# Optimization experiments

Measured on AMD Instinct MI355X. Metric: run time of the kernel, lower is better.

Reference implementation:

```python
import jax, jax.numpy as jnp
import numpy as np

A, B, NB = 100_000, 200_000, 6      # atoms, directed bonds, max neighbors
FA, FB, H = 133, 147, 256            # atom fdim, bond fdim, hidden
M, DEPTH = 5_000, 4                  # molecules, message-passing depth


def setup_inputs() -> dict:
    key = jax.random.key(0)
    ks = jax.random.split(key, 12)
    f_atoms = jax.random.normal(ks[0], (A, FA), jnp.float32)
    f_bonds = jax.random.normal(ks[1], (B, FB), jnp.float32)
    a2b = jax.random.randint(ks[2], (A, NB), 0, B, dtype=jnp.int32)
    b2a = jax.random.randint(ks[3], (B,), 0, A, dtype=jnp.int32)
    b2revb = jax.random.randint(ks[4], (B,), 0, B, dtype=jnp.int32)
    # weights (bias=False per args.bias, except W_o which always has bias)
    W_ia = jax.random.normal(ks[5], (FA, H), jnp.float32) / np.sqrt(FA)
    W_ib = jax.random.normal(ks[6], (FB, H), jnp.float32) / np.sqrt(FB)
    W_h = jax.random.normal(ks[7], (DEPTH - 1, H, H), jnp.float32) / np.sqrt(H)
    W_o = jax.random.normal(ks[8], (H, H), jnp.float32) / np.sqrt(H)
    b_o = jax.random.normal(ks[9], (H,), jnp.float32) * 0.01
    W_lr = jax.random.normal(ks[10], (3 * H, H), jnp.float32) / np.sqrt(3 * H)
    # ragged molecule sizes summing exactly to A (avg 20 atoms/mol)
    rng = np.random.default_rng(0)
    sizes = (A // M) + rng.integers(-5, 6, M)
    sizes[-1] += A - sizes.sum()
    sizes = jnp.asarray(sizes, jnp.int32)
    return dict(f_atoms=f_atoms, f_bonds=f_bonds, W_ia=W_ia, W_ib=W_ib,
                W_h=W_h, W_o=W_o, b_o=b_o, W_lr=W_lr,
                a2b=a2b, b2a=b2a, b2revb=b2revb, sizes=sizes)


def _sum_max_agg(message_bond, a2b):
    nei = message_bond[a2b]                 # [A, NB, H] gather
    return nei.sum(axis=1) * nei.max(axis=1)


def reference(f_atoms, f_bonds, W_ia, W_ib, W_h, W_o, b_o, W_lr,
              a2b, b2a, b2revb, sizes):
    input_atom = jax.nn.relu(f_atoms @ W_ia)    # [A, H]
    message_atom = input_atom
    input_bond = jax.nn.relu(f_bonds @ W_ib)    # [B, H]
    message_bond = input_bond
    for d in range(DEPTH - 1):
        agg = _sum_max_agg(message_bond, a2b)          # [A, H]
        message_atom = message_atom + agg
        rev = message_bond[b2revb]                     # [B, H]
        message_bond = message_atom[b2a] - rev
        message_bond = jax.nn.relu(input_bond + message_bond @ W_h[d])
        # dropout p=0.0 -> identity
    agg = _sum_max_agg(message_bond, a2b)              # [A, H]
    agg = jnp.concatenate([agg, message_atom, input_atom], axis=1) @ W_lr
    atom_hiddens = jax.nn.relu(agg @ W_o + b_o)        # [A, H]
    # ragged per-molecule mean pooling (a_scope)
    mol_ids = jnp.repeat(jnp.arange(M), sizes, total_repeat_length=A)
    sums = jax.ops.segment_sum(atom_hiddens, mol_ids, num_segments=M)
    mol_vecs = sums / sizes[:, None].astype(atom_hiddens.dtype)
    return mol_vecs                                    # [M, H]
```

## Files before the change

### kernel.cpp

```cpp
#include <hip/hip_runtime.h>


typedef _Float16 f16;
typedef f16 f16x4 __attribute__((ext_vector_type(4)));
typedef f16 f16x8 __attribute__((ext_vector_type(8)));
typedef __attribute__((ext_vector_type(8))) short bh8;
typedef __attribute__((ext_vector_type(4))) float f32x4;

#define MB_SCALE 0.000244140625f
#define MB_INV   4096.0f
#define AGG_INV  16777216.0f

__device__ __forceinline__ unsigned short f2bf_rne(float f) {
    unsigned u = __float_as_uint(f);
    unsigned r = (u + 0x7fffu + ((u >> 16) & 1u)) >> 16;
    return (unsigned short)r;
}
__device__ __forceinline__ float bfu2f(unsigned short u) {
    return __uint_as_float(((unsigned)u) << 16);
}
__device__ __forceinline__ f32x4 mfma16(bh8 a, bh8 b, f32x4 c) {
    return __builtin_amdgcn_mfma_f32_16x16x32_bf16(a, b, c, 0, 0, 0);
}

__global__ __launch_bounds__(256) void wprep_kernel(
    const float* __restrict__ Wia, const float* __restrict__ Wib,
    const float* __restrict__ Wh,  const float* __restrict__ Wlr,
    const float* __restrict__ Wo,  short* __restrict__ ws)
{
    short* WiaT_hi = ws;
    short* WiaT_lo = ws + 40960;
    short* WibT_hi = ws + 81920;
    short* WibT_lo = ws + 122880;
    short* WhT_hi  = ws + 163840;
    short* WhT_lo  = ws + 360448;
    short* WlrT_hi = ws + 557056;
    short* WlrT_lo = ws + 753664;
    short* WoT_hi  = ws + 950272;
    short* WoT_lo  = ws + 1015808;

    int idx = blockIdx.x * 256 + threadIdx.x;
    float v; short *ph, *pl; int o;
    if (idx < 40960) {
        int n = idx / 160, k = idx - n * 160;
        v = (k < 133) ? Wia[(size_t)k * 256 + n] : 0.f;
        ph = WiaT_hi; pl = WiaT_lo; o = idx;
    } else if (idx < 81920) {
        int j = idx - 40960;
        int n = j / 160, k = j - n * 160;
        v = (k < 147) ? Wib[(size_t)k * 256 + n] : 0.f;
        ph = WibT_hi; pl = WibT_lo; o = j;
    } else if (idx < 278528) {
        int j = idx - 81920;
        int d = j >> 16, rem = j & 65535, n = rem >> 8, k = rem & 255;
        v = Wh[(size_t)d * 65536 + (size_t)k * 256 + n];
        ph = WhT_hi; pl = WhT_lo; o = j;
    } else if (idx < 475136) {
        int j = idx - 278528;
        int n = j / 768, k = j - n * 768;
        v = Wlr[(size_t)k * 256 + n];
        ph = WlrT_hi; pl = WlrT_lo; o = j;
    } else if (idx < 540672) {
        int j = idx - 475136;
        int n = j >> 8, k = j & 255;
        v = Wo[(size_t)k * 256 + n];
        ph = WoT_hi; pl = WoT_lo; o = j;
    } else return;
    unsigned short hb = f2bf_rne(v);
    ph[o] = (short)hb;
    pl[o] = (short)f2bf_rne(v - bfu2f(hb));
}

template <int KPAD, int SRC, int EPI>
__global__ __launch_bounds__(512, 4) void mfma_gemm(
    const void* __restrict__ a0, const void* __restrict__ a1,
    const void* __restrict__ a2,
    const short* __restrict__ Bhi, const short* __restrict__ Blo,
    const float* __restrict__ bias, void* __restrict__ outv,
    int M, int Kact)
{
    __shared__ short As_hi[128 * 40];
    __shared__ short As_lo[(SRC == 2) ? 8 : 128 * 40];

    const int tid  = threadIdx.x;
    const int lane = tid & 63;
    const int w    = tid >> 6;
    const int wm   = (w >> 2) * 64;
    const int wn   = (w & 3) * 64;
    const int row0 = blockIdx.x * 128;

    const int sm = tid >> 2;
    const int sk = (tid & 3) * 8;
    const int fm = lane & 15;
    const int fk = (lane >> 4) * 8;

    int grow = row0 + sm; if (grow > M - 1) grow = M - 1;

    f32x4 acc[4][4];
#pragma unroll
    for (int i = 0; i < 4; ++i)
#pragma unroll
        for (int j = 0; j < 4; ++j) {
            f32x4 z = {0.f, 0.f, 0.f, 0.f};
            acc[i][j] = z;
        }

    for (int k0 = 0; k0 < KPAD; k0 += 32) {
        __syncthreads();
        int base = sm * 40 + sk;
        if (SRC == 0) {
            const float* xrow = (const float*)a0 + (size_t)grow * Kact;
            bh8 h0, l0;
#pragma unroll
            for (int j = 0; j < 8; ++j) {
                int kc = k0 + sk + j;
                float v = (kc < Kact) ? xrow[kc] : 0.f;
                unsigned short hb = f2bf_rne(v);
                h0[j] = (short)hb; l0[j] = (short)f2bf_rne(v - bfu2f(hb));
            }
            *(bh8*)&As_hi[base] = h0;
            *(bh8*)&As_lo[base] = l0;
        } else if (SRC == 1) {
            if (k0 < 512) {
                const float* src = (k0 < 256) ? (const float*)a0 : (const float*)a1;
                int kl = k0 & 255;
                const float4* p = (const float4*)(src + (size_t)grow * 256 + kl + sk);
                float va[8];
#pragma unroll
                for (int q = 0; q < 2; ++q) {
                    float4 f = p[q];
                    va[q * 4 + 0] = f.x; va[q * 4 + 1] = f.y;
                    va[q * 4 + 2] = f.z; va[q * 4 + 3] = f.w;
                }
                bh8 h0, l0;
#pragma unroll
                for (int j = 0; j < 8; ++j) {
                    unsigned short hb = f2bf_rne(va[j]);
                    h0[j] = (short)hb; l0[j] = (short)f2bf_rne(va[j] - bfu2f(hb));
                }
                *(bh8*)&As_hi[base] = h0;
                *(bh8*)&As_lo[base] = l0;
            } else {
                const short* ia = (const short*)a2 + (size_t)grow * 256 + (k0 - 512) + sk;
                bh8 z;
#pragma unroll
                for (int j = 0; j < 8; ++j) z[j] = 0;
                *(bh8*)&As_hi[base] = *(const bh8*)ia;
                *(bh8*)&As_lo[base] = z;
            }
        } else {
            const short* xr = (const short*)a0 + (size_t)grow * 256 + k0 + sk;
            *(bh8*)&As_hi[base] = *(const bh8*)xr;
        }
        __syncthreads();

        bh8 bhf[4], blf[4];
#pragma unroll
        for (int nt = 0; nt < 4; ++nt) {
            int n = wn + nt * 16 + fm;
            size_t off = (size_t)n * KPAD + k0 + fk;
            bhf[nt] = *(const bh8*)(Bhi + off);
            blf[nt] = *(const bh8*)(Blo + off);
        }
#pragma unroll
        for (int mt = 0; mt < 4; ++mt) {
            int abase = (wm + mt * 16 + fm) * 40 + fk;
            bh8 ah = *(const bh8*)&As_hi[abase];
#pragma unroll
            for (int nt = 0; nt < 4; ++nt) {
                acc[mt][nt] = mfma16(ah, bhf[nt], acc[mt][nt]);
                acc[mt][nt] = mfma16(ah, blf[nt], acc[mt][nt]);
            }
            if (SRC != 2) {
                bh8 al = *(const bh8*)&As_lo[abase];
#pragma unroll
                for (int nt = 0; nt < 4; ++nt)
                    acc[mt][nt] = mfma16(al, bhf[nt], acc[mt][nt]);
            }
        }
    }

#pragma unroll
    for (int mt = 0; mt < 4; ++mt) {
        int rbase = row0 + wm + mt * 16 + (lane >> 4) * 4;
#pragma unroll
        for (int nt = 0; nt < 4; ++nt) {
            int col = wn + nt * 16 + fm;
            float bc = (EPI == 4) ? bias[col] : 0.f;
#pragma unroll
            for (int r = 0; r < 4; ++r) {
                int row = rbase + r;
                if (row < M) {
                    size_t o = (size_t)row * 256 + col;
                    float v = acc[mt][nt][r];
                    if (EPI == 0)      ((float*)outv)[o] = fmaxf(v, 0.f);
                    else if (EPI == 1) ((unsigned short*)outv)[o] = f2bf_rne(fmaxf(v, 0.f));
                    else if (EPI == 2) ((f16*)outv)[o] = (f16)(fmaxf(v, 0.f) * MB_SCALE);
                    else if (EPI == 3) ((unsigned short*)outv)[o] = f2bf_rne(v);
                    else               ((float*)outv)[o] = fmaxf(v + bc, 0.f);
                }
            }
        }
    }
}

template <bool WITH_FB>
__global__ __launch_bounds__(512, 4) void bond_mfma_kernel(
    const float* __restrict__ FB,
    const short* __restrict__ WibT_hi, const short* __restrict__ WibT_lo,
    const short* __restrict__ WhT_hi,  const short* __restrict__ WhT_lo,
    const float* __restrict__ matom, const f16* __restrict__ mb_old,
    const f16* ib,
    const int* __restrict__ b2a, const int* __restrict__ b2revb,
    f16* mb_new, int M)
{
    __shared__ short As[2][2][128 * 40];

    const int tid  = threadIdx.x;
    const int lane = tid & 63;
    const int w    = tid >> 6;
    const int wm   = (w >> 2) * 64;
    const int wn   = (w & 3) * 64;
    const int row0 = blockIdx.x * 128;

    const int sm = tid >> 2;
    const int sk = (tid & 3) * 8;

    int grow = row0 + sm; if (grow > M - 1) grow = M - 1;
    const float* frow = FB + (size_t)grow * 147;
    const float* arow = matom + (size_t)b2a[grow] * 256;
    const f16*   rrow = mb_old + (size_t)b2revb[grow] * 256;

    const int fm = lane & 15;
    const int fk = (lane >> 4) * 8;

    f32x4 acc[4][4];
#pragma unroll
    for (int i = 0; i < 4; ++i)
#pragma unroll
        for (int j = 0; j < 4; ++j) {
            f32x4 z = {0.f, 0.f, 0.f, 0.f};
            acc[i][j] = z;
        }

    float va[8];

    auto load = [&](int s) {
        if (s < 5) {
            int kb = s * 32 + sk;
#pragma unroll
            for (int j = 0; j < 8; ++j) {
                int kc = kb + j;
                va[j] = (kc < 147) ? frow[kc] : 0.f;
            }
        } else {
            int kb = (s - 5) * 32 + sk;
            const float4* ap = (const float4*)(arow + kb);
            const f16x4*  rp = (const f16x4*)(rrow + kb);
#pragma unroll
            for (int q = 0; q < 2; ++q) {
                float4 a = ap[q]; f16x4 r = rp[q];
                va[q * 4 + 0] = fmaf(-MB_INV, (float)r[0], a.x);
                va[q * 4 + 1] = fmaf(-MB_INV, (float)r[1], a.y);
                va[q * 4 + 2] = fmaf(-MB_INV, (float)r[2], a.z);
                va[q * 4 + 3] = fmaf(-MB_INV, (float)r[3], a.w);
            }
        }
    };
    auto store = [&](int buf) {
        bh8 h, l;
#pragma unroll
        for (int j = 0; j < 8; ++j) {
            unsigned short hb = f2bf_rne(va[j]);
            h[j] = (short)hb;
            l[j] = (short)f2bf_rne(va[j] - bfu2f(hb));
        }
        int base = sm * 40 + sk;
        *(bh8*)&As[buf][0][base] = h;
        *(bh8*)&As[buf][1][base] = l;
    };
    auto compute = [&](int buf, int s) {
        const short *Bh, *Bl; int ldb, k0;
        if (s < 5) { Bh = WibT_hi; Bl = WibT_lo; ldb = 160; k0 = s * 32; }
        else       { Bh = WhT_hi;  Bl = WhT_lo;  ldb = 256; k0 = (s - 5) * 32; }
        bh8 bhf[4], blf[4];
#pragma unroll
        for (int nt = 0; nt < 4; ++nt) {
            int n = wn + nt * 16 + fm;
            size_t off = (size_t)n * ldb + k0 + fk;
            bhf[nt] = *(const bh8*)(Bh + off);
            blf[nt] = *(const bh8*)(Bl + off);
        }
#pragma unroll
        for (int mt = 0; mt < 4; ++mt) {
            int abase = (wm + mt * 16 + fm) * 40 + fk;
            bh8 ah = *(const bh8*)&As[buf][0][abase];
            bh8 al = *(const bh8*)&As[buf][1][abase];
#pragma unroll
            for (int nt = 0; nt < 4; ++nt) {
                acc[mt][nt] = mfma16(ah, bhf[nt], acc[mt][nt]);
                acc[mt][nt] = mfma16(ah, blf[nt], acc[mt][nt]);
                acc[mt][nt] = mfma16(al, bhf[nt], acc[mt][nt]);
            }
        }
    };

    const int S0 = WITH_FB ? 0 : 5;

    load(S0);
    store(0);
    __syncthreads();

    int cur = 0;
    for (int s = S0; s < 13; ++s) {
        if (s < 12) load(s + 1);
        compute(cur, s);
        if (WITH_FB && s == 4) {
#pragma unroll
            for (int i = 0; i < 4; ++i)
#pragma unroll
                for (int j = 0; j < 4; ++j)
#pragma unroll
                    for (int r = 0; r < 4; ++r)
                        acc[i][j][r] = fmaxf(acc[i][j][r], 0.f);
        }
        if (s < 12) store(cur ^ 1);
        __syncthreads();
        cur ^= 1;
    }

#pragma unroll
    for (int mt = 0; mt < 4; ++mt) {
        int rbase = row0 + wm + mt * 16 + (lane >> 4) * 4;
#pragma unroll
        for (int nt = 0; nt < 4; ++nt) {
            int col = wn + nt * 16 + fm;
#pragma unroll
            for (int r = 0; r < 4; ++r) {
                int row = rbase + r;
                if (row < M) {
                    size_t o = (size_t)row * 256 + col;
                    float v = acc[mt][nt][r];
                    if (!WITH_FB) v = fmaf(MB_INV, (float)ib[o], v);
                    mb_new[o] = (f16)(fmaxf(v, 0.f) * MB_SCALE);
                }
            }
        }
    }
}

__global__ __launch_bounds__(256) void agg_kernel(
    const f16* __restrict__ mb, const int* __restrict__ a2b,
    float* __restrict__ matom, float* __restrict__ agg_out, int A)
{
    const int a    = blockIdx.x * 4 + (threadIdx.x >> 6);
    const int lane = threadIdx.x & 63;
    if (a >= A) return;
    const int* nb = a2b + (size_t)a * 6;

    f16x4 v0 = *(const f16x4*)(mb + (size_t)nb[0] * 256 + lane * 4);
    float s0 = (float)v0[0], s1 = (float)v0[1], s2 = (float)v0[2], s3 = (float)v0[3];
    float m0 = s0, m1 = s1, m2 = s2, m3 = s3;
#pragma unroll
    for (int j = 1; j < 6; ++j) {
        f16x4 v = *(const f16x4*)(mb + (size_t)nb[j] * 256 + lane * 4);
        float f0 = (float)v[0], f1 = (float)v[1], f2 = (float)v[2], f3 = (float)v[3];
        s0 += f0; s1 += f1; s2 += f2; s3 += f3;
        m0 = fmaxf(m0, f0); m1 = fmaxf(m1, f1);
        m2 = fmaxf(m2, f2); m3 = fmaxf(m3, f3);
    }
    size_t o = (size_t)a * 256 + lane * 4;
    if (agg_out) {
        float4 g = { AGG_INV * s0 * m0, AGG_INV * s1 * m1,
                     AGG_INV * s2 * m2, AGG_INV * s3 * m3 };
        *(float4*)(agg_out + o) = g;
    } else {
        float4 m = *(const float4*)(matom + o);
        m.x += AGG_INV * s0 * m0; m.y += AGG_INV * s1 * m1;
        m.z += AGG_INV * s2 * m2; m.w += AGG_INV * s3 * m3;
        *(float4*)(matom + o) = m;
    }
}

__global__ __launch_bounds__(256) void scan_kernel(
    const int* __restrict__ sizes, int* __restrict__ offsets, int M)
{
    __shared__ int part[256];
    const int t = threadIdx.x;
    const int chunk = (M + 255) / 256;
    int begin = t * chunk;
    int end = begin + chunk; if (end > M) end = M;
    int s = 0;
    for (int i = begin; i < end && i < M; ++i) s += sizes[i];
    part[t] = s;
    __syncthreads();
    for (int off = 1; off < 256; off <<= 1) {
        int v = (t >= off) ? part[t - off] : 0;
        __syncthreads();
        part[t] += v;
        __syncthreads();
    }
    int run = part[t] - s;
    for (int i = begin; i < end && i < M; ++i) { offsets[i] = run; run += sizes[i]; }
}

__global__ __launch_bounds__(256) void pool_kernel(
    const float* __restrict__ hid, const int* __restrict__ offsets,
    const int* __restrict__ sizes, float* __restrict__ out, int M, int A)
{
    const int m = blockIdx.x;
    const int h = threadIdx.x;
    int e = offsets[m];
    int sz = sizes[m];
    int start = e < A ? e : A;          if (start < 0) start = 0;
    int stop  = e + sz; if (stop > A) stop = A; if (stop < 0) stop = 0;
    float s = 0.f;
    for (int i = start; i < stop; ++i)
        s += hid[(size_t)i * 256 + h];
    out[(size_t)m * 256 + h] = s / (float)sz;
}

extern "C" void kernel_launch(void* const* d_in, const int* in_sizes, int n_in,
                              void* d_out, int out_size, void* d_ws, size_t ws_size,
                              hipStream_t stream)
{
    const float* f_atoms = (const float*)d_in[0];
    const float* f_bonds = (const float*)d_in[1];
    const float* W_ia    = (const float*)d_in[2];
    const float* W_ib    = (const float*)d_in[3];
    const float* W_h     = (const float*)d_in[4];
    const float* W_o     = (const float*)d_in[5];
    const float* b_o     = (const float*)d_in[6];
    const float* W_lr    = (const float*)d_in[7];
    const int*   a2b     = (const int*)d_in[8];
    const int*   b2a     = (const int*)d_in[9];
    const int*   b2revb  = (const int*)d_in[10];
    const int*   sizes   = (const int*)d_in[11];
    float* out = (float*)d_out;

    const int An = 100000, Bn = 200000, Mm = 5000;
    const size_t ABYTES = (size_t)An * 256 * 4;
    const size_t BBYTES = (size_t)Bn * 256 * 2;

    int*   offsets = (int*)d_ws;
    float* matom   = (float*)((char*)d_ws + 32768);
    f16*   mb0     = (f16*)((char*)matom + ABYTES);
    f16*   mb1     = (f16*)((char*)mb0 + BBYTES);
    short* wsplit  = (short*)((char*)mb1 + BBYTES);

    short* WiaT_hi = wsplit;
    short* WiaT_lo = wsplit + 40960;
    short* WibT_hi = wsplit + 81920;
    short* WibT_lo = wsplit + 122880;
    short* WhT_hi  = wsplit + 163840;
    short* WhT_lo  = wsplit + 360448;
    short* WlrT_hi = wsplit + 557056;
    short* WlrT_lo = wsplit + 753664;
    short* WoT_hi  = wsplit + 950272;
    short* WoT_lo  = wsplit + 1015808;

    dim3 blk(256);
    dim3 blk512(512);
    dim3 gA((An + 127) / 128, 1);
    dim3 gB((Bn + 127) / 128, 1);

    wprep_kernel<<<2112, blk, 0, stream>>>(W_ia, W_ib, W_h, W_lr, W_o, wsplit);

    mfma_gemm<160, 0, 0><<<gA, blk512, 0, stream>>>(
        f_atoms, nullptr, nullptr, WiaT_hi, WiaT_lo, nullptr, matom, An, 133);
    mfma_gemm<160, 0, 2><<<gB, blk512, 0, stream>>>(
        f_bonds, nullptr, nullptr, WibT_hi, WibT_lo, nullptr, mb0, Bn, 147);

    agg_kernel<<<(An + 3) / 4, blk, 0, stream>>>(mb0, a2b, matom, (float*)nullptr, An);
    bond_mfma_kernel<false><<<gB, blk512, 0, stream>>>(
        f_bonds, WibT_hi, WibT_lo, WhT_hi, WhT_lo,
        matom, mb0, mb0, b2a, b2revb, mb1, Bn);
    agg_kernel<<<(An + 3) / 4, blk, 0, stream>>>(mb1, a2b, matom, (float*)nullptr, An);
    bond_mfma_kernel<false><<<gB, blk512, 0, stream>>>(
        f_bonds, WibT_hi, WibT_lo, WhT_hi + 65536, WhT_lo + 65536,
        matom, mb1, mb0, b2a, b2revb, mb0, Bn);
    agg_kernel<<<(An + 3) / 4, blk, 0, stream>>>(mb0, a2b, matom, (float*)nullptr, An);
    bond_mfma_kernel<true><<<gB, blk512, 0, stream>>>(
        f_bonds, WibT_hi, WibT_lo, WhT_hi + 131072, WhT_lo + 131072,
        matom, mb0, nullptr, b2a, b2revb, mb1, Bn);

    float* aggbuf = (float*)mb0;
    agg_kernel<<<(An + 3) / 4, blk, 0, stream>>>(mb1, a2b, matom, aggbuf, An);

    unsigned short* iatom = (unsigned short*)mb1;
    unsigned short* t1    = (unsigned short*)((char*)mb1 + 51200000);
    mfma_gemm<160, 0, 1><<<gA, blk512, 0, stream>>>(
        f_atoms, nullptr, nullptr, WiaT_hi, WiaT_lo, nullptr, iatom, An, 133);

    mfma_gemm<768, 1, 3><<<gA, blk512, 0, stream>>>(
        aggbuf, matom, iatom, WlrT_hi, WlrT_lo, nullptr, t1, An, 768);

    float* hid = (float*)mb0;
    mfma_gemm<256, 2, 4><<<gA, blk512, 0, stream>>>(
        t1, nullptr, nullptr, WoT_hi, WoT_lo, b_o, hid, An, 256);

    scan_kernel<<<1, 256, 0, stream>>>(sizes, offsets, Mm);
    pool_kernel<<<Mm, blk, 0, stream>>>(hid, offsets, sizes, out, Mm, An);
}
```

Measured before the change: 1.822 ms.

## Prefetch bond-kernel gather two stages ahead with register double-buffering

Rewrites the bond MFMA kernel's main loop so global loads for the atom message and reverse-bond message are issued two k-stages ahead into alternating register sets, instead of one stage ahead. This gives the gathers more time to land before they are needed. It also pads the LDS row stride from 40 to 44 shorts to change the bank-conflict pattern, fully unrolls the stage loop, and loads B fragments in pairs of n-tiles to reduce register pressure. The extra register buffers may hurt occupancy under the 512x4 launch bounds.

```diff
diff --git a/kernel.cpp b/kernel.cpp
--- a/kernel.cpp
+++ b/kernel.cpp
@@ -204,6 +204,77 @@
     }
 }
 
+#define BOND_ISSUE_G(A0, A1, RR, t) {                                        \
+    int kb_ = ((t) - 5) * 32 + sk;                                           \
+    A0 = *(const float4*)(arow + kb_);                                       \
+    A1 = *(const float4*)(arow + kb_ + 4);                                   \
+    RR = *(const f16x8*)(rrow + kb_);                                        \
+}
+#define BOND_ISSUE_F(A0, A1, t) {                                            \
+    int kb_ = (t) * 32 + sk;                                                 \
+    float t0_ = (kb_ + 0 < 147) ? frow[kb_ + 0] : 0.f;                       \
+    float t1_ = (kb_ + 1 < 147) ? frow[kb_ + 1] : 0.f;                       \
+    float t2_ = (kb_ + 2 < 147) ? frow[kb_ + 2] : 0.f;                       \
+    float t3_ = (kb_ + 3 < 147) ? frow[kb_ + 3] : 0.f;                       \
+    float t4_ = (kb_ + 4 < 147) ? frow[kb_ + 4] : 0.f;                       \
+    float t5_ = (kb_ + 5 < 147) ? frow[kb_ + 5] : 0.f;                       \
+    float t6_ = (kb_ + 6 < 147) ? frow[kb_ + 6] : 0.f;                       \
+    float t7_ = (kb_ + 7 < 147) ? frow[kb_ + 7] : 0.f;                       \
+    A0 = make_float4(t0_, t1_, t2_, t3_);                                    \
+    A1 = make_float4(t4_, t5_, t6_, t7_);                                    \
+}
+#define BOND_SPLIT8(V0,V1,V2,V3,V4,V5,V6,V7, buf) {                          \
+    bh8 h_, l_;                                                              \
+    unsigned short hb_;                                                      \
+    hb_ = f2bf_rne(V0); h_[0] = (short)hb_; l_[0] = (short)f2bf_rne(V0 - bfu2f(hb_)); \
+    hb_ = f2bf_rne(V1); h_[1] = (short)hb_; l_[1] = (short)f2bf_rne(V1 - bfu2f(hb_)); \
+    hb_ = f2bf_rne(V2); h_[2] = (short)hb_; l_[2] = (short)f2bf_rne(V2 - bfu2f(hb_)); \
+    hb_ = f2bf_rne(V3); h_[3] = (short)hb_; l_[3] = (short)f2bf_rne(V3 - bfu2f(hb_)); \
+    hb_ = f2bf_rne(V4); h_[4] = (short)hb_; l_[4] = (short)f2bf_rne(V4 - bfu2f(hb_)); \
+    hb_ = f2bf_rne(V5); h_[5] = (short)hb_; l_[5] = (short)f2bf_rne(V5 - bfu2f(hb_)); \
+    hb_ = f2bf_rne(V6); h_[6] = (short)hb_; l_[6] = (short)f2bf_rne(V6 - bfu2f(hb_)); \
+    hb_ = f2bf_rne(V7); h_[7] = (short)hb_; l_[7] = (short)f2bf_rne(V7 - bfu2f(hb_)); \
+    *(bh8*)&As[buf][0][lbase] = h_;                                          \
+    *(bh8*)&As[buf][1][lbase] = l_;                                          \
+}
+#define BOND_STORE_G(A0, A1, RR, buf) {                                      \
+    float v0_ = fmaf(-MB_INV, (float)RR[0], A0.x);                           \
+    float v1_ = fmaf(-MB_INV, (float)RR[1], A0.y);                           \
+    float v2_ = fmaf(-MB_INV, (float)RR[2], A0.z);                           \
+    float v3_ = fmaf(-MB_INV, (float)RR[3], A0.w);                           \
+    float v4_ = fmaf(-MB_INV, (float)RR[4], A1.x);                           \
+    float v5_ = fmaf(-MB_INV, (float)RR[5], A1.y);                           \
+    float v6_ = fmaf(-MB_INV, (float)RR[6], A1.z);                           \
+    float v7_ = fmaf(-MB_INV, (float)RR[7], A1.w);                           \
+    BOND_SPLIT8(v0_, v1_, v2_, v3_, v4_, v5_, v6_, v7_, buf)                 \
+}
+#define BOND_STORE_F(A0, A1, buf) {                                          \
+    BOND_SPLIT8(A0.x, A0.y, A0.z, A0.w, A1.x, A1.y, A1.z, A1.w, buf)         \
+}
+#define BOND_COMPUTE(buf, Bh, Bl, ldb, k0) {                                 \
+    _Pragma("unroll")                                                        \
+    for (int g_ = 0; g_ < 2; ++g_) {                                         \
+        size_t o0_ = (size_t)(wn + (g_ * 2 + 0) * 16 + fm) * (ldb) + (k0) + fk; \
+        size_t o1_ = (size_t)(wn + (g_ * 2 + 1) * 16 + fm) * (ldb) + (k0) + fk; \
+        bh8 b0h_ = *(const bh8*)((Bh) + o0_);                                \
+        bh8 b0l_ = *(const bh8*)((Bl) + o0_);                                \
+        bh8 b1h_ = *(const bh8*)((Bh) + o1_);                                \
+        bh8 b1l_ = *(const bh8*)((Bl) + o1_);                                \
+        _Pragma("unroll")                                                    \
+        for (int mt_ = 0; mt_ < 4; ++mt_) {                                  \
+            int ab_ = (wm + mt_ * 16 + fm) * 44 + fk;                        \
+            bh8 ah_ = *(const bh8*)&As[buf][0][ab_];                         \
+            bh8 al_ = *(const bh8*)&As[buf][1][ab_];                         \
+            acc[mt_][g_ * 2 + 0] = mfma16(ah_, b0h_, acc[mt_][g_ * 2 + 0]);  \
+            acc[mt_][g_ * 2 + 0] = mfma16(ah_, b0l_, acc[mt_][g_ * 2 + 0]);  \
+            acc[mt_][g_ * 2 + 0] = mfma16(al_, b0h_, acc[mt_][g_ * 2 + 0]);  \
+            acc[mt_][g_ * 2 + 1] = mfma16(ah_, b1h_, acc[mt_][g_ * 2 + 1]);  \
+            acc[mt_][g_ * 2 + 1] = mfma16(ah_, b1l_, acc[mt_][g_ * 2 + 1]);  \
+            acc[mt_][g_ * 2 + 1] = mfma16(al_, b1h_, acc[mt_][g_ * 2 + 1]);  \
+        }                                                                    \
+    }                                                                        \
+}
+
 template <bool WITH_FB>
 __global__ __launch_bounds__(512, 4) void bond_mfma_kernel(
     const float* __restrict__ FB,
@@ -214,7 +285,7 @@
     const int* __restrict__ b2a, const int* __restrict__ b2revb,
     f16* mb_new, int M)
 {
-    __shared__ short As[2][2][128 * 40];
+    __shared__ short As[2][2][128 * 44];
 
     const int tid  = threadIdx.x;
     const int lane = tid & 63;
@@ -225,6 +296,7 @@
 
     const int sm = tid >> 2;
     const int sk = (tid & 3) * 8;
+    const int lbase = sm * 44 + sk;
 
     int grow = row0 + sm; if (grow > M - 1) grow = M - 1;
     const float* frow = FB + (size_t)grow * 147;
@@ -243,78 +315,39 @@
             acc[i][j] = z;
         }
 
-    float va[8];
-
-    auto load = [&](int s) {
-        if (s < 5) {
-            int kb = s * 32 + sk;
-#pragma unroll
-            for (int j = 0; j < 8; ++j) {
-                int kc = kb + j;
-                va[j] = (kc < 147) ? frow[kc] : 0.f;
-            }
+    float4 xa0, xa1; f16x8 xr;
+    float4 ya0, ya1; f16x8 yr;
+
+    const int S0 = WITH_FB ? 0 : 5;
+
+    if (WITH_FB) {
+        BOND_ISSUE_F(xa0, xa1, 0)
+        BOND_STORE_F(xa0, xa1, 0)
+        BOND_ISSUE_F(ya0, ya1, 1)
+    } else {
+        BOND_ISSUE_G(ya0, ya1, yr, 5)
+        BOND_STORE_G(ya0, ya1, yr, 0)
+        BOND_ISSUE_G(xa0, xa1, xr, 6)
+    }
+    __syncthreads();
+
+#pragma unroll
+    for (int s = S0; s <= 12; ++s) {
+        const int buf = (s - S0) & 1;
+        if (s + 2 <= 12) {
+            if ((s & 1) == 0) {
+                if (WITH_FB && (s + 2) < 5) { BOND_ISSUE_F(xa0, xa1, s + 2) }
+                else                        { BOND_ISSUE_G(xa0, xa1, xr, s + 2) }
+            } else {
+                if (WITH_FB && (s + 2) < 5) { BOND_ISSUE_F(ya0, ya1, s + 2) }
+                else                        { BOND_ISSUE_G(ya0, ya1, yr, s + 2) }
+            }
+        }
+        if (WITH_FB && s < 5) {
+            BOND_COMPUTE(buf, WibT_hi, WibT_lo, 160, s * 32)
         } else {
-            int kb = (s - 5) * 32 + sk;
-            const float4* ap = (const float4*)(arow + kb);
-            const f16x4*  rp = (const f16x4*)(rrow + kb);
-#pragma unroll
-            for (int q = 0; q < 2; ++q) {
-                float4 a = ap[q]; f16x4 r = rp[q];
-                va[q * 4 + 0] = fmaf(-MB_INV, (float)r[0], a.x);
-                va[q * 4 + 1] = fmaf(-MB_INV, (float)r[1], a.y);
-                va[q * 4 + 2] = fmaf(-MB_INV, (float)r[2], a.z);
-                va[q * 4 + 3] = fmaf(-MB_INV, (float)r[3], a.w);
-            }
-        }
-    };
-    auto store = [&](int buf) {
-        bh8 h, l;
-#pragma unroll
-        for (int j = 0; j < 8; ++j) {
-            unsigned short hb = f2bf_rne(va[j]);
-            h[j] = (short)hb;
-            l[j] = (short)f2bf_rne(va[j] - bfu2f(hb));
-        }
-        int base = sm * 40 + sk;
-        *(bh8*)&As[buf][0][base] = h;
-        *(bh8*)&As[buf][1][base] = l;
-    };
-    auto compute = [&](int buf, int s) {
-        const short *Bh, *Bl; int ldb, k0;
-        if (s < 5) { Bh = WibT_hi; Bl = WibT_lo; ldb = 160; k0 = s * 32; }
-        else       { Bh = WhT_hi;  Bl = WhT_lo;  ldb = 256; k0 = (s - 5) * 32; }
-        bh8 bhf[4], blf[4];
-#pragma unroll
-        for (int nt = 0; nt < 4; ++nt) {
-            int n = wn + nt * 16 + fm;
-            size_t off = (size_t)n * ldb + k0 + fk;
-            bhf[nt] = *(const bh8*)(Bh + off);
-            blf[nt] = *(const bh8*)(Bl + off);
-        }
-#pragma unroll
-        for (int mt = 0; mt < 4; ++mt) {
-            int abase = (wm + mt * 16 + fm) * 40 + fk;
-            bh8 ah = *(const bh8*)&As[buf][0][abase];
-            bh8 al = *(const bh8*)&As[buf][1][abase];
-#pragma unroll
-            for (int nt = 0; nt < 4; ++nt) {
-                acc[mt][nt] = mfma16(ah, bhf[nt], acc[mt][nt]);
-                acc[mt][nt] = mfma16(ah, blf[nt], acc[mt][nt]);
-                acc[mt][nt] = mfma16(al, bhf[nt], acc[mt][nt]);
-            }
-        }
-    };
-
-    const int S0 = WITH_FB ? 0 : 5;
-
-    load(S0);
-    store(0);
-    __syncthreads();
-
-    int cur = 0;
-    for (int s = S0; s < 13; ++s) {
-        if (s < 12) load(s + 1);
-        compute(cur, s);
+            BOND_COMPUTE(buf, WhT_hi, WhT_lo, 256, (s - 5) * 32)
+        }
         if (WITH_FB && s == 4) {
 #pragma unroll
             for (int i = 0; i < 4; ++i)
@@ -324,9 +357,16 @@
                     for (int r = 0; r < 4; ++r)
                         acc[i][j][r] = fmaxf(acc[i][j][r], 0.f);
         }
-        if (s < 12) store(cur ^ 1);
-        __syncthreads();
-        cur ^= 1;
+        if (s < 12) {
+            if (((s + 1) & 1) == 0) {
+                if (WITH_FB && (s + 1) < 5) { BOND_STORE_F(xa0, xa1, buf ^ 1) }
+                else                        { BOND_STORE_G(xa0, xa1, xr, buf ^ 1) }
+            } else {
+                if (WITH_FB && (s + 1) < 5) { BOND_STORE_F(ya0, ya1, buf ^ 1) }
+                else                        { BOND_STORE_G(ya0, ya1, yr, buf ^ 1) }
+            }
+            __syncthreads();
+        }
     }
 
 #pragma unroll
```

Result: slower. 2.151 ms (+18.0%).
